# Optimization experiments

Measured on AMD Instinct MI355X. Metric: run time of the kernel, lower is better.

Reference implementation:

```python
import jax, jax.numpy as jnp
import numpy as np

N = 50000
E = 400000
D_IN = 128
D_OUT = 128
D_NODE = 6
EPS = 1e-5


def _layernorm(h, g, b):
    mu = jnp.mean(h, axis=-1, keepdims=True)
    var = jnp.var(h, axis=-1, keepdims=True)
    return (h - mu) * jax.lax.rsqrt(var + EPS) * g + b


def setup_inputs() -> dict:
    key = jax.random.key(0)
    ks = jax.random.split(key, 8)
    d_cat = 3 * D_IN + 2 * D_NODE  # 396 = input_dim*3 + 12
    return {
        "x": jax.random.normal(ks[0], (N, D_NODE), jnp.float32),
        "edge_index": jax.random.randint(ks[1], (2, E), 0, N, dtype=jnp.int32),
        "edge_attr": jax.random.normal(ks[2], (E, D_IN), jnp.float32),
        "mask": (jax.random.uniform(ks[3], (E,)) > 0.5).astype(jnp.float32),
        "num_nodes": N,
        "W_edge": jax.random.normal(ks[4], (d_cat, D_OUT), jnp.float32) / np.sqrt(d_cat).astype(np.float32),
        "b_edge": jnp.zeros((D_OUT,), jnp.float32),
        "W1": jax.random.normal(ks[5], (D_OUT, 2 * D_OUT), jnp.float32) / np.sqrt(D_OUT).astype(np.float32),
        "b1": jnp.zeros((2 * D_OUT,), jnp.float32),
        "W2": jax.random.normal(ks[6], (2 * D_OUT, D_OUT), jnp.float32) / np.sqrt(2 * D_OUT).astype(np.float32),
        "b2": jnp.zeros((D_OUT,), jnp.float32),
        "g1": jnp.ones((D_OUT,), jnp.float32),
        "be1": jnp.zeros((D_OUT,), jnp.float32),
        "g2": jnp.ones((D_OUT,), jnp.float32),
        "be2": jnp.zeros((D_OUT,), jnp.float32),
    }


def reference(x, edge_attr, mask, W_edge, b_edge, W1, b1, W2, b2, g1, be1, g2, be2, edge_index, num_nodes):
    row, col = edge_index[0], edge_index[1]
    # mean-like aggregation of incoming edge features onto destination nodes
    agg = jax.ops.segment_sum(edge_attr * mask[:, None], col, num_segments=num_nodes)  # [N, D_IN]
    den = jax.ops.segment_sum(mask, col, num_segments=num_nodes) + 1.0  # [N]
    node_rep = jnp.concatenate([agg / den[:, None], x], axis=1)  # [N, D_IN + D_NODE]
    edge_rep = jnp.concatenate([node_rep[row], node_rep[col], edge_attr], axis=-1)  # [E, 3*D_IN+12]
    h = _layernorm(edge_attr[:, :D_OUT] + edge_rep @ W_edge + b_edge, g1, be1)  # [E, D_OUT]
    out = _layernorm(h + jax.nn.relu(h @ W1 + b1) @ W2 + b2, g2, be2)  # [E, D_OUT]
    return (node_rep, out)
```

## Files before the change

### kernel.cpp

```cpp
#include <hip/hip_runtime.h>


constexpr int NN = 50000;
constexpr int NE = 400000;
constexpr int DI = 128;
constexpr int DN = 6;
constexpr int DR = 134;
constexpr float LN_EPS = 1e-5f;

using f4 = __attribute__((ext_vector_type(4))) float;
using s8 = __attribute__((ext_vector_type(8))) short;

__device__ __forceinline__ unsigned short f2bf(float f) {
    unsigned u = __float_as_uint(f);
    u += 0x7fff + ((u >> 16) & 1);
    return (unsigned short)(u >> 16);
}

__device__ __forceinline__ float bf2f(unsigned short b) {
    return __uint_as_float((unsigned)b << 16);
}

__device__ __forceinline__ float red16(float v) {
    int x;
    x = __builtin_amdgcn_update_dpp(0, __float_as_int(v), 0x121, 0xf, 0xf, true);
    v += __int_as_float(x);
    x = __builtin_amdgcn_update_dpp(0, __float_as_int(v), 0x122, 0xf, 0xf, true);
    v += __int_as_float(x);
    x = __builtin_amdgcn_update_dpp(0, __float_as_int(v), 0x124, 0xf, 0xf, true);
    v += __int_as_float(x);
    x = __builtin_amdgcn_update_dpp(0, __float_as_int(v), 0x128, 0xf, 0xf, true);
    v += __int_as_float(x);
    return v;
}

__global__ __launch_bounds__(256) void deg_kernel(
    const float* __restrict__ mask, const int* __restrict__ ei,
    int* __restrict__ deg)
{
    int e = blockIdx.x * 256 + threadIdx.x;
    if (e >= NE) return;
    if (mask[e] != 0.f) atomicAdd(&deg[ei[NE + e]], 1);
}

__global__ __launch_bounds__(1024) void scan_kernel(
    const int* __restrict__ deg, int* __restrict__ offs, int* __restrict__ cursor)
{
    __shared__ int part[1024];
    const int t = threadIdx.x;
    constexpr int CH = (NN + 1023) / 1024;
    const int base = t * CH;
    const int lim  = min(base + CH, NN);

    int s = 0;
    for (int i = base; i < lim; ++i) s += deg[i];
    part[t] = s;
    __syncthreads();
    for (int off = 1; off < 1024; off <<= 1) {
        int add = (t >= off) ? part[t - off] : 0;
        __syncthreads();
        part[t] += add;
        __syncthreads();
    }
    int run = (t == 0) ? 0 : part[t - 1];
    for (int i = base; i < lim; ++i) {
        offs[i]   = run;
        cursor[i] = run;
        run += deg[i];
    }
    if (t == 1023) offs[NN] = part[1023];
}

__global__ __launch_bounds__(256) void binfill_kernel(
    const float* __restrict__ mask, const int* __restrict__ ei,
    int* __restrict__ cursor, int* __restrict__ bucket)
{
    int e = blockIdx.x * 256 + threadIdx.x;
    if (e >= NE) return;
    if (mask[e] != 0.f) {
        int pos = atomicAdd(&cursor[ei[NE + e]], 1);
        bucket[pos] = e;
    }
}

__global__ __launch_bounds__(256) void gather_kernel(
    const float* __restrict__ edge_attr, const float* __restrict__ x,
    const int* __restrict__ offs, const int* __restrict__ bucket,
    float* __restrict__ node_out)
{
    int n = blockIdx.x * 4 + (threadIdx.x >> 6);
    if (n >= NN) return;
    const int lane = threadIdx.x & 63;
    const int beg = offs[n], end = offs[n + 1];
    float2 acc = make_float2(0.f, 0.f);
    for (int j = beg; j < end; ++j) {
        int e = bucket[j];
        float2 v = *reinterpret_cast<const float2*>(edge_attr + (size_t)e * 128 + lane * 2);
        acc.x += v.x;
        acc.y += v.y;
    }
    float inv = 1.f / (float)(end - beg + 1);
    float2 o = make_float2(acc.x * inv, acc.y * inv);
    *reinterpret_cast<float2*>(node_out + (size_t)n * DR + lane * 2) = o;
    if (lane < DN) node_out[(size_t)n * DR + DI + lane] = x[n * DN + lane];
}

__global__ __launch_bounds__(256) void prep_w_kernel(
    const float* __restrict__ W_edge, const float* __restrict__ W1,
    const float* __restrict__ W2,
    unsigned short* __restrict__ WcT, unsigned short* __restrict__ W1T,
    unsigned short* __restrict__ W2T)
{
    int idx = blockIdx.x * 256 + threadIdx.x;
    if (idx < 16384) {
        int n = idx >> 7, k = idx & 127;
        float v = W_edge[(268 + k) * 128 + n] + (k == n ? 1.f : 0.f);
        WcT[n * 128 + k] = f2bf(v);
    } else if (idx < 49152) {
        int j = idx - 16384;
        int n = j >> 7, k = j & 127;
        W1T[n * 128 + k] = f2bf(W1[k * 256 + n]);
    } else if (idx < 81920) {
        int j = idx - 49152;
        int n = j >> 8, k = j & 255;
        W2T[n * 256 + k] = f2bf(W2[k * 128 + n]);
    }
}

__global__ __launch_bounds__(256) void pq_kernel(
    const float* __restrict__ nr, const float* __restrict__ W_edge,
    const float* __restrict__ b_edge,
    float* __restrict__ P, float* __restrict__ Q)
{
    __shared__ float As[64 * 136];
    const int t = threadIdx.x;
    const int n0 = blockIdx.x * 64;

    for (int idx = t; idx < 64 * 136; idx += 256) {
        int n = idx / 136, k = idx - n * 136;
        float v = 0.f;
        if (n0 + n < NN && k < DR) v = nr[(size_t)(n0 + n) * DR + k];
        As[idx] = v;
    }
    __syncthreads();

    const int et = t >> 5, jt = t & 31;
    float4 accP[8], accQ[8];
    #pragma unroll
    for (int i = 0; i < 8; ++i) {
        accP[i] = make_float4(0.f, 0.f, 0.f, 0.f);
        accQ[i] = make_float4(0.f, 0.f, 0.f, 0.f);
    }
    for (int k0 = 0; k0 < 136; k0 += 4) {
        float4 wa[4], wb[4];
        #pragma unroll
        for (int d = 0; d < 4; ++d) {
            wa[d] = *reinterpret_cast<const float4*>(&W_edge[(size_t)(k0 + d) * 128 + 4 * jt]);
            wb[d] = *reinterpret_cast<const float4*>(&W_edge[(size_t)(134 + k0 + d) * 128 + 4 * jt]);
        }
        #pragma unroll
        for (int i = 0; i < 8; ++i) {
            float4 a4 = *reinterpret_cast<const float4*>(&As[(8 * et + i) * 136 + k0]);
            accP[i].x += a4.x * wa[0].x + a4.y * wa[1].x + a4.z * wa[2].x + a4.w * wa[3].x;
            accP[i].y += a4.x * wa[0].y + a4.y * wa[1].y + a4.z * wa[2].y + a4.w * wa[3].y;
            accP[i].z += a4.x * wa[0].z + a4.y * wa[1].z + a4.z * wa[2].z + a4.w * wa[3].z;
            accP[i].w += a4.x * wa[0].w + a4.y * wa[1].w + a4.z * wa[2].w + a4.w * wa[3].w;
            accQ[i].x += a4.x * wb[0].x + a4.y * wb[1].x + a4.z * wb[2].x + a4.w * wb[3].x;
            accQ[i].y += a4.x * wb[0].y + a4.y * wb[1].y + a4.z * wb[2].y + a4.w * wb[3].y;
            accQ[i].z += a4.x * wb[0].z + a4.y * wb[1].z + a4.z * wb[2].z + a4.w * wb[3].z;
            accQ[i].w += a4.x * wb[0].w + a4.y * wb[1].w + a4.z * wb[2].w + a4.w * wb[3].w;
        }
    }
    float4 bev = *reinterpret_cast<const float4*>(&b_edge[4 * jt]);
    #pragma unroll
    for (int i = 0; i < 8; ++i) {
        int n = n0 + 8 * et + i;
        if (n < NN) {
            float4 p = accP[i];
            p.x += bev.x; p.y += bev.y; p.z += bev.z; p.w += bev.w;
            *reinterpret_cast<float4*>(&P[(size_t)n * 128 + 4 * jt]) = p;
            *reinterpret_cast<float4*>(&Q[(size_t)n * 128 + 4 * jt]) = accQ[i];
        }
    }
}

constexpr int ET = 32;
constexpr int NTILE = NE / ET;
constexpr int FFN_GRID = 512;

__global__ __launch_bounds__(512, 4) void ffn_kernel(
    const float* __restrict__ edge_attr,
    const int* __restrict__ ei,
    const float* __restrict__ P,
    const float* __restrict__ Q,
    const unsigned short* __restrict__ WcT,
    const unsigned short* __restrict__ W1T,
    const unsigned short* __restrict__ W2T,
    const float* __restrict__ b1, const float* __restrict__ b2,
    const float* __restrict__ g1, const float* __restrict__ be1,
    const float* __restrict__ g2, const float* __restrict__ be2,
    float* __restrict__ out)
{
    __shared__ short lds_a[ET * 128];
    __shared__ short lds_u[ET * 256];
    __shared__ float red_part[8][ET][2];

    const int t    = threadIdx.x;
    const int w    = t >> 6;
    const int lane = t & 63;
    const int q    = lane >> 4;
    const int c    = lane & 15;
    const int cw   = w;

    s8 wcf[4], w1f[2][4], w2f[8];
    #pragma unroll
    for (int k0 = 0; k0 < 4; ++k0)
        wcf[k0] = *reinterpret_cast<const s8*>(WcT + (cw * 16 + c) * 128 + k0 * 32 + q * 8);
    #pragma unroll
    for (int nt = 0; nt < 2; ++nt)
        #pragma unroll
        for (int k0 = 0; k0 < 4; ++k0)
            w1f[nt][k0] = *reinterpret_cast<const s8*>(W1T + (cw * 32 + nt * 16 + c) * 128 + k0 * 32 + q * 8);
    #pragma unroll
    for (int k0 = 0; k0 < 8; ++k0)
        w2f[k0] = *reinterpret_cast<const s8*>(W2T + (cw * 16 + c) * 256 + k0 * 32 + q * 8);

    const float g1c  = g1[cw * 16 + c],  be1c = be1[cw * 16 + c];
    const float b1v0 = b1[cw * 32 + c],  b1v1 = b1[cw * 32 + 16 + c];
    const float b2c  = b2[cw * 16 + c];
    const float g2c  = g2[cw * 16 + c],  be2c = be2[cw * 16 + c];

    const int srow = t >> 4;
    const int sti  = t & 15;

    for (int tile = blockIdx.x; tile < NTILE; tile += gridDim.x) {
        const int e0 = tile * ET;

        {
            const float4* src = reinterpret_cast<const float4*>(
                edge_attr + (size_t)(e0 + srow) * 128 + sti * 8);
            float4 v0 = src[0], v1 = src[1];
            s8 bb;
            bb[0] = (short)f2bf(v0.x); bb[1] = (short)f2bf(v0.y);
            bb[2] = (short)f2bf(v0.z); bb[3] = (short)f2bf(v0.w);
            bb[4] = (short)f2bf(v1.x); bb[5] = (short)f2bf(v1.y);
            bb[6] = (short)f2bf(v1.z); bb[7] = (short)f2bf(v1.w);
            *reinterpret_cast<s8*>(&lds_a[srow * 128 + (sti ^ (srow & 7)) * 8]) = bb;
        }
        __syncthreads();

        f4 acc1[2];
        acc1[0] = {0.f, 0.f, 0.f, 0.f};
        acc1[1] = {0.f, 0.f, 0.f, 0.f};
        #pragma unroll
        for (int k0 = 0; k0 < 4; ++k0)
            #pragma unroll
            for (int mt = 0; mt < 2; ++mt) {
                s8 a = *reinterpret_cast<const s8*>(
                    &lds_a[(mt * 16 + c) * 128 + ((k0 * 4 + q) ^ (c & 7)) * 8]);
                acc1[mt] = __builtin_amdgcn_mfma_f32_16x16x32_bf16(a, wcf[k0], acc1[mt], 0, 0, 0);
            }

        #pragma unroll
        for (int mt = 0; mt < 2; ++mt)
            #pragma unroll
            for (int reg = 0; reg < 4; ++reg) {
                int e  = e0 + mt * 16 + q * 4 + reg;
                int er = ei[e], ec = ei[NE + e];
                acc1[mt][reg] += P[(size_t)er * 128 + cw * 16 + c]
                               + Q[(size_t)ec * 128 + cw * 16 + c];
            }

        #pragma unroll
        for (int mt = 0; mt < 2; ++mt)
            #pragma unroll
            for (int reg = 0; reg < 4; ++reg) {
                float v  = acc1[mt][reg];
                float sv = red16(v);
                float sq = red16(v * v);
                if (c == 0) {
                    int r = mt * 16 + q * 4 + reg;
                    float2 p2; p2.x = sv; p2.y = sq;
                    *reinterpret_cast<float2*>(&red_part[cw][r][0]) = p2;
                }
            }
        __syncthreads();

        float mu_l = 0.f, rs_l = 0.f;
        if (lane < ET) {
            float s = 0.f, ss = 0.f;
            #pragma unroll
            for (int i = 0; i < 8; ++i) {
                float2 p2 = *reinterpret_cast<const float2*>(&red_part[i][lane][0]);
                s += p2.x; ss += p2.y;
            }
            mu_l = s * (1.f / 128.f);
            float var = ss * (1.f / 128.f) - mu_l * mu_l;
            rs_l = rsqrtf(var + LN_EPS);
        }

        #pragma unroll
        for (int mt = 0; mt < 2; ++mt)
            #pragma unroll
            for (int reg = 0; reg < 4; ++reg) {
                int r = mt * 16 + q * 4 + reg;
                float mu = __shfl(mu_l, r, 64);
                float rs = __shfl(rs_l, r, 64);
                float h = (acc1[mt][reg] - mu) * rs * g1c + be1c;
                lds_a[r * 128 + ((cw * 2 + (c >> 3)) ^ (r & 7)) * 8 + (c & 7)] = (short)f2bf(h);
            }
        __syncthreads();

        f4 acc2[2][2];
        acc2[0][0] = {0.f,0.f,0.f,0.f}; acc2[0][1] = {0.f,0.f,0.f,0.f};
        acc2[1][0] = {0.f,0.f,0.f,0.f}; acc2[1][1] = {0.f,0.f,0.f,0.f};
        #pragma unroll
        for (int k0 = 0; k0 < 4; ++k0)
            #pragma unroll
            for (int mt = 0; mt < 2; ++mt) {
                s8 a = *reinterpret_cast<const s8*>(
                    &lds_a[(mt * 16 + c) * 128 + ((k0 * 4 + q) ^ (c & 7)) * 8]);
                acc2[mt][0] = __builtin_amdgcn_mfma_f32_16x16x32_bf16(a, w1f[0][k0], acc2[mt][0], 0, 0, 0);
                acc2[mt][1] = __builtin_amdgcn_mfma_f32_16x16x32_bf16(a, w1f[1][k0], acc2[mt][1], 0, 0, 0);
            }
        #pragma unroll
        for (int mt = 0; mt < 2; ++mt)
            #pragma unroll
            for (int reg = 0; reg < 4; ++reg) {
                int r = mt * 16 + q * 4 + reg;
                float u0 = fmaxf(acc2[mt][0][reg] + b1v0, 0.f);
                float u1 = fmaxf(acc2[mt][1][reg] + b1v1, 0.f);
                int ch0 = (cw * 4 + (c >> 3)) ^ (r & 7);
                int ch1 = (cw * 4 + 2 + (c >> 3)) ^ (r & 7);
                lds_u[r * 256 + ch0 * 8 + (c & 7)] = (short)f2bf(u0);
                lds_u[r * 256 + ch1 * 8 + (c & 7)] = (short)f2bf(u1);
            }
        __syncthreads();

        f4 acc3[2];
        #pragma unroll
        for (int mt = 0; mt < 2; ++mt)
            #pragma unroll
            for (int reg = 0; reg < 4; ++reg) {
                int r = mt * 16 + q * 4 + reg;
                acc3[mt][reg] = bf2f((unsigned short)
                    lds_a[r * 128 + ((cw * 2 + (c >> 3)) ^ (r & 7)) * 8 + (c & 7)]) + b2c;
            }
        #pragma unroll
        for (int k0 = 0; k0 < 8; ++k0)
            #pragma unroll
            for (int mt = 0; mt < 2; ++mt) {
                s8 a = *reinterpret_cast<const s8*>(
                    &lds_u[(mt * 16 + c) * 256 + ((k0 * 4 + q) ^ (c & 7)) * 8]);
                acc3[mt] = __builtin_amdgcn_mfma_f32_16x16x32_bf16(a, w2f[k0], acc3[mt], 0, 0, 0);
            }

        #pragma unroll
        for (int mt = 0; mt < 2; ++mt)
            #pragma unroll
            for (int reg = 0; reg < 4; ++reg) {
                float v  = acc3[mt][reg];
                float sv = red16(v);
                float sq = red16(v * v);
                if (c == 0) {
                    int r = mt * 16 + q * 4 + reg;
                    float2 p2; p2.x = sv; p2.y = sq;
                    *reinterpret_cast<float2*>(&red_part[cw][r][0]) = p2;
                }
            }
        __syncthreads();

        float mu2_l = 0.f, rs2_l = 0.f;
        if (lane < ET) {
            float s = 0.f, ss = 0.f;
            #pragma unroll
            for (int i = 0; i < 8; ++i) {
                float2 p2 = *reinterpret_cast<const float2*>(&red_part[i][lane][0]);
                s += p2.x; ss += p2.y;
            }
            mu2_l = s * (1.f / 128.f);
            float var = ss * (1.f / 128.f) - mu2_l * mu2_l;
            rs2_l = rsqrtf(var + LN_EPS);
        }

        #pragma unroll
        for (int mt = 0; mt < 2; ++mt)
            #pragma unroll
            for (int reg = 0; reg < 4; ++reg) {
                int r = mt * 16 + q * 4 + reg;
                float mu = __shfl(mu2_l, r, 64);
                float rs = __shfl(rs2_l, r, 64);
                float o = (acc3[mt][reg] - mu) * rs * g2c + be2c;
                out[(size_t)(e0 + r) * 128 + cw * 16 + c] = o;
            }
    }
}

extern "C" void kernel_launch(void* const* d_in, const int* in_sizes, int n_in,
                              void* d_out, int out_size, void* d_ws, size_t ws_size,
                              hipStream_t stream) {
    const float* x         = (const float*)d_in[0];
    const int*   ei        = (const int*)  d_in[1];
    const float* edge_attr = (const float*)d_in[2];
    const float* mask      = (const float*)d_in[3];
    const float* W_edge    = (const float*)d_in[5];
    const float* b_edge    = (const float*)d_in[6];
    const float* W1        = (const float*)d_in[7];
    const float* b1        = (const float*)d_in[8];
    const float* W2        = (const float*)d_in[9];
    const float* b2        = (const float*)d_in[10];
    const float* g1        = (const float*)d_in[11];
    const float* be1       = (const float*)d_in[12];
    const float* g2        = (const float*)d_in[13];
    const float* be2       = (const float*)d_in[14];

    float* node_out  = (float*)d_out;
    float* out_edges = (float*)d_out + (size_t)NN * DR;

    char* ws = (char*)d_ws;
    int*            deg    = (int*)(ws);
    int*            offs   = (int*)(ws + (256 << 10));
    int*            cursor = (int*)(ws + (512 << 10));
    unsigned short* WcT    = (unsigned short*)(ws + (768 << 10));
    unsigned short* W1T    = (unsigned short*)(ws + (768 << 10) + 32768);
    unsigned short* W2T    = (unsigned short*)(ws + (768 << 10) + 98304);
    int*            bucket = (int*)(ws + (1 << 20));
    float*          P      = (float*)(ws + (1 << 20));
    float*          Q      = (float*)(ws + (1 << 20) + 26214400);

    hipMemsetAsync(deg, 0, (size_t)NN * sizeof(int), stream);

    deg_kernel<<<(NE + 255) / 256, 256, 0, stream>>>(mask, ei, deg);
    scan_kernel<<<1, 1024, 0, stream>>>(deg, offs, cursor);
    binfill_kernel<<<(NE + 255) / 256, 256, 0, stream>>>(mask, ei, cursor, bucket);
    gather_kernel<<<(NN + 3) / 4, 256, 0, stream>>>(edge_attr, x, offs, bucket, node_out);
    prep_w_kernel<<<320, 256, 0, stream>>>(W_edge, W1, W2, WcT, W1T, W2T);
    pq_kernel<<<(NN + 63) / 64, 256, 0, stream>>>(node_out, W_edge, b_edge, P, Q);
    ffn_kernel<<<FFN_GRID, 512, 0, stream>>>(edge_attr, ei, P, Q, WcT, W1T, W2T,
                                             b1, b2, g1, be1, g2, be2, out_edges);
}
```

Baseline: 1.019 ms.

## Double FFN tile to 64 edges with 1024 threads and prefetch P/Q gathers

```diff
diff --git a/kernel.cpp b/kernel.cpp
--- a/kernel.cpp
+++ b/kernel.cpp
@@ -19,6 +19,13 @@
 
 __device__ __forceinline__ float bf2f(unsigned short b) {
     return __uint_as_float((unsigned)b << 16);
+}
+
+__device__ __forceinline__ void bar_lds() {
+    __builtin_amdgcn_sched_barrier(0);
+    asm volatile("s_waitcnt lgkmcnt(0)" ::: "memory");
+    __builtin_amdgcn_s_barrier();
+    __builtin_amdgcn_sched_barrier(0);
 }
 
 __device__ __forceinline__ float red16(float v) {
@@ -184,11 +191,11 @@
     }
 }
 
-constexpr int ET = 32;
+constexpr int ET = 64;
 constexpr int NTILE = NE / ET;
-constexpr int FFN_GRID = 512;
-
-__global__ __launch_bounds__(512, 4) void ffn_kernel(
+constexpr int FFN_GRID = 256;
+
+__global__ __launch_bounds__(1024, 4) void ffn_kernel(
     const float* __restrict__ edge_attr,
     const int* __restrict__ ei,
     const float* __restrict__ P,
@@ -203,14 +210,15 @@
 {
     __shared__ short lds_a[ET * 128];
     __shared__ short lds_u[ET * 256];
-    __shared__ float red_part[8][ET][2];
+    __shared__ float red_part[2][8][32][2];
 
     const int t    = threadIdx.x;
     const int w    = t >> 6;
     const int lane = t & 63;
     const int q    = lane >> 4;
     const int c    = lane & 15;
-    const int cw   = w;
+    const int mg   = w >> 3;
+    const int cw   = w & 7;
 
     s8 wcf[4], w1f[2][4], w2f[8];
     #pragma unroll
@@ -235,6 +243,25 @@
 
     for (int tile = blockIdx.x; tile < NTILE; tile += gridDim.x) {
         const int e0 = tile * ET;
+        const int eb = e0 + mg * 32;
+
+        int er[2][4], ec[2][4];
+        #pragma unroll
+        for (int mt = 0; mt < 2; ++mt)
+            #pragma unroll
+            for (int reg = 0; reg < 4; ++reg) {
+                int e = eb + mt * 16 + q * 4 + reg;
+                er[mt][reg] = ei[e];
+                ec[mt][reg] = ei[NE + e];
+            }
+        float pr[2][4], qr[2][4];
+        #pragma unroll
+        for (int mt = 0; mt < 2; ++mt)
+            #pragma unroll
+            for (int reg = 0; reg < 4; ++reg) {
+                pr[mt][reg] = P[(size_t)er[mt][reg] * 128 + cw * 16 + c];
+                qr[mt][reg] = Q[(size_t)ec[mt][reg] * 128 + cw * 16 + c];
+            }
 
         {
             const float4* src = reinterpret_cast<const float4*>(
@@ -247,7 +274,7 @@
             bb[6] = (short)f2bf(v1.z); bb[7] = (short)f2bf(v1.w);
             *reinterpret_cast<s8*>(&lds_a[srow * 128 + (sti ^ (srow & 7)) * 8]) = bb;
         }
-        __syncthreads();
+        bar_lds();
 
         f4 acc1[2];
         acc1[0] = {0.f, 0.f, 0.f, 0.f};
@@ -257,19 +284,15 @@
             #pragma unroll
             for (int mt = 0; mt < 2; ++mt) {
                 s8 a = *reinterpret_cast<const s8*>(
-                    &lds_a[(mt * 16 + c) * 128 + ((k0 * 4 + q) ^ (c & 7)) * 8]);
+                    &lds_a[(mg * 32 + mt * 16 + c) * 128 + ((k0 * 4 + q) ^ (c & 7)) * 8]);
                 acc1[mt] = __builtin_amdgcn_mfma_f32_16x16x32_bf16(a, wcf[k0], acc1[mt], 0, 0, 0);
             }
 
         #pragma unroll
         for (int mt = 0; mt < 2; ++mt)
             #pragma unroll
-            for (int reg = 0; reg < 4; ++reg) {
-                int e  = e0 + mt * 16 + q * 4 + reg;
-                int er = ei[e], ec = ei[NE + e];
-                acc1[mt][reg] += P[(size_t)er * 128 + cw * 16 + c]
-                               + Q[(size_t)ec * 128 + cw * 16 + c];
-            }
+            for (int reg = 0; reg < 4; ++reg)
+                acc1[mt][reg] += pr[mt][reg] + qr[mt][reg];
 
         #pragma unroll
         for (int mt = 0; mt < 2; ++mt)
@@ -281,17 +304,17 @@
                 if (c == 0) {
                     int r = mt * 16 + q * 4 + reg;
                     float2 p2; p2.x = sv; p2.y = sq;
-                    *reinterpret_cast<float2*>(&red_part[cw][r][0]) = p2;
+                    *reinterpret_cast<float2*>(&red_part[mg][cw][r][0]) = p2;
                 }
             }
-        __syncthreads();
+        bar_lds();
 
         float mu_l = 0.f, rs_l = 0.f;
-        if (lane < ET) {
+        if (lane < 32) {
             float s = 0.f, ss = 0.f;
             #pragma unroll
             for (int i = 0; i < 8; ++i) {
-                float2 p2 = *reinterpret_cast<const float2*>(&red_part[i][lane][0]);
+                float2 p2 = *reinterpret_cast<const float2*>(&red_part[mg][i][lane][0]);
                 s += p2.x; ss += p2.y;
             }
             mu_l = s * (1.f / 128.f);
@@ -303,13 +326,14 @@
         for (int mt = 0; mt < 2; ++mt)
             #pragma unroll
             for (int reg = 0; reg < 4; ++reg) {
-                int r = mt * 16 + q * 4 + reg;
+                int r  = mt * 16 + q * 4 + reg;
+                int gr = mg * 32 + r;
                 float mu = __shfl(mu_l, r, 64);
                 float rs = __shfl(rs_l, r, 64);
                 float h = (acc1[mt][reg] - mu) * rs * g1c + be1c;
-                lds_a[r * 128 + ((cw * 2 + (c >> 3)) ^ (r & 7)) * 8 + (c & 7)] = (short)f2bf(h);
-            }
-        __syncthreads();
+                lds_a[gr * 128 + ((cw * 2 + (c >> 3)) ^ (r & 7)) * 8 + (c & 7)] = (short)f2bf(h);
+            }
+        bar_lds();
 
         f4 acc2[2][2];
         acc2[0][0] = {0.f,0.f,0.f,0.f}; acc2[0][1] = {0.f,0.f,0.f,0.f};
@@ -319,7 +343,7 @@
             #pragma unroll
             for (int mt = 0; mt < 2; ++mt) {
                 s8 a = *reinterpret_cast<const s8*>(
-                    &lds_a[(mt * 16 + c) * 128 + ((k0 * 4 + q) ^ (c & 7)) * 8]);
+                    &lds_a[(mg * 32 + mt * 16 + c) * 128 + ((k0 * 4 + q) ^ (c & 7)) * 8]);
                 acc2[mt][0] = __builtin_amdgcn_mfma_f32_16x16x32_bf16(a, w1f[0][k0], acc2[mt][0], 0, 0, 0);
                 acc2[mt][1] = __builtin_amdgcn_mfma_f32_16x16x32_bf16(a, w1f[1][k0], acc2[mt][1], 0, 0, 0);
             }
@@ -327,31 +351,33 @@
         for (int mt = 0; mt < 2; ++mt)
             #pragma unroll
             for (int reg = 0; reg < 4; ++reg) {
-                int r = mt * 16 + q * 4 + reg;
+                int r  = mt * 16 + q * 4 + reg;
+                int gr = mg * 32 + r;
                 float u0 = fmaxf(acc2[mt][0][reg] + b1v0, 0.f);
                 float u1 = fmaxf(acc2[mt][1][reg] + b1v1, 0.f);
                 int ch0 = (cw * 4 + (c >> 3)) ^ (r & 7);
                 int ch1 = (cw * 4 + 2 + (c >> 3)) ^ (r & 7);
-                lds_u[r * 256 + ch0 * 8 + (c & 7)] = (short)f2bf(u0);
-                lds_u[r * 256 + ch1 * 8 + (c & 7)] = (short)f2bf(u1);
-            }
-        __syncthreads();
+                lds_u[gr * 256 + ch0 * 8 + (c & 7)] = (short)f2bf(u0);
+                lds_u[gr * 256 + ch1 * 8 + (c & 7)] = (short)f2bf(u1);
+            }
+        bar_lds();
 
         f4 acc3[2];
         #pragma unroll
         for (int mt = 0; mt < 2; ++mt)
             #pragma unroll
             for (int reg = 0; reg < 4; ++reg) {
-                int r = mt * 16 + q * 4 + reg;
+                int r  = mt * 16 + q * 4 + reg;
+                int gr = mg * 32 + r;
                 acc3[mt][reg] = bf2f((unsigned short)
-                    lds_a[r * 128 + ((cw * 2 + (c >> 3)) ^ (r & 7)) * 8 + (c & 7)]) + b2c;
+                    lds_a[gr * 128 + ((cw * 2 + (c >> 3)) ^ (r & 7)) * 8 + (c & 7)]) + b2c;
             }
         #pragma unroll
         for (int k0 = 0; k0 < 8; ++k0)
             #pragma unroll
             for (int mt = 0; mt < 2; ++mt) {
                 s8 a = *reinterpret_cast<const s8*>(
-                    &lds_u[(mt * 16 + c) * 256 + ((k0 * 4 + q) ^ (c & 7)) * 8]);
+                    &lds_u[(mg * 32 + mt * 16 + c) * 256 + ((k0 * 4 + q) ^ (c & 7)) * 8]);
                 acc3[mt] = __builtin_amdgcn_mfma_f32_16x16x32_bf16(a, w2f[k0], acc3[mt], 0, 0, 0);
             }
 
@@ -365,17 +391,17 @@
                 if (c == 0) {
                     int r = mt * 16 + q * 4 + reg;
                     float2 p2; p2.x = sv; p2.y = sq;
-                    *reinterpret_cast<float2*>(&red_part[cw][r][0]) = p2;
+                    *reinterpret_cast<float2*>(&red_part[mg][cw][r][0]) = p2;
                 }
             }
-        __syncthreads();
+        bar_lds();
 
         float mu2_l = 0.f, rs2_l = 0.f;
-        if (lane < ET) {
+        if (lane < 32) {
             float s = 0.f, ss = 0.f;
             #pragma unroll
             for (int i = 0; i < 8; ++i) {
-                float2 p2 = *reinterpret_cast<const float2*>(&red_part[i][lane][0]);
+                float2 p2 = *reinterpret_cast<const float2*>(&red_part[mg][i][lane][0]);
                 s += p2.x; ss += p2.y;
             }
             mu2_l = s * (1.f / 128.f);
@@ -387,11 +413,12 @@
         for (int mt = 0; mt < 2; ++mt)
             #pragma unroll
             for (int reg = 0; reg < 4; ++reg) {
-                int r = mt * 16 + q * 4 + reg;
+                int r  = mt * 16 + q * 4 + reg;
+                int gr = mg * 32 + r;
                 float mu = __shfl(mu2_l, r, 64);
                 float rs = __shfl(rs2_l, r, 64);
                 float o = (acc3[mt][reg] - mu) * rs * g2c + be2c;
-                out[(size_t)(e0 + r) * 128 + cw * 16 + c] = o;
+                out[(size_t)(e0 + gr) * 128 + cw * 16 + c] = o;
             }
     }
 }
@@ -436,6 +463,6 @@
     gather_kernel<<<(NN + 3) / 4, 256, 0, stream>>>(edge_attr, x, offs, bucket, node_out);
     prep_w_kernel<<<320, 256, 0, stream>>>(W_edge, W1, W2, WcT, W1T, W2T);
     pq_kernel<<<(NN + 63) / 64, 256, 0, stream>>>(node_out, W_edge, b_edge, P, Q);
-    ffn_kernel<<<FFN_GRID, 512, 0, stream>>>(edge_attr, ei, P, Q, WcT, W1T, W2T,
-                                             b1, b2, g1, be1, g2, be2, out_edges);
-}
+    ffn_kernel<<<FFN_GRID, 1024, 0, stream>>>(edge_attr, ei, P, Q, WcT, W1T, W2T,
+                                              b1, b2, g1, be1, g2, be2, out_edges);
+}
```

Measured after the change: 1.138 ms. 11.7% more time.
